# Kernel optimization log

Measured on AMD Instinct MI355X. Metric: run time of the kernel, lower is better.

## Reference

```python
import jax, jax.numpy as jnp
import numpy as np

N_NODES = 100000
N_EDGES = 1600000
F_IN_N = 64
F_IN_E = 64
F_OUT_N = 64
F_OUT_E = 64


def setup_inputs() -> dict:
    key = jax.random.key(0)
    ks = jax.random.split(key, 10)
    nfeats = jax.random.normal(ks[0], (N_NODES, F_IN_N), dtype=jnp.float32)
    efeats = jax.random.normal(ks[1], (N_EDGES, F_IN_E), dtype=jnp.float32)
    src = jax.random.randint(ks[2], (N_EDGES,), 0, N_NODES, dtype=jnp.int32)
    dst = jax.random.randint(ks[3], (N_EDGES,), 0, N_NODES, dtype=jnp.int32)
    s = 0.05
    W_node = jax.random.normal(ks[4], (F_OUT_N, F_IN_N), dtype=jnp.float32) * s
    b_node = jnp.zeros((F_OUT_N,), dtype=jnp.float32)
    W_ni = jax.random.normal(ks[5], (F_OUT_E, F_IN_N), dtype=jnp.float32) * s
    W_nj = jax.random.normal(ks[6], (F_OUT_E, F_IN_N), dtype=jnp.float32) * s
    W_fij = jax.random.normal(ks[7], (F_OUT_E, F_IN_E), dtype=jnp.float32) * s
    bias = jnp.zeros((F_OUT_E,), dtype=jnp.float32)
    return {"nfeats": nfeats, "efeats": efeats, "src": src, "dst": dst,
            "W_node": W_node, "b_node": b_node, "W_ni": W_ni, "W_nj": W_nj,
            "W_fij": W_fij, "bias": bias}


def reference(nfeats, efeats, src, dst, W_node, b_node, W_ni, W_nj, W_fij, bias):
    # edge update: leaky_relu(f_ni[src] + f_nj[dst] + f_fij + bias)
    f_ni = nfeats @ W_ni.T        # [N, Fe]
    f_nj = nfeats @ W_nj.T        # [N, Fe]
    f_fij = efeats @ W_fij.T      # [E, Fe]
    f_out = jax.nn.leaky_relu(f_ni[src] + f_nj[dst] + f_fij + bias, negative_slope=0.01)
    # node update: mean over in-edges of transformed source features
    h = nfeats @ W_node.T + b_node                      # [N, Fn]
    msg_sum = jax.ops.segment_sum(h[src], dst, num_segments=N_NODES)   # [N, Fn]
    deg = jax.ops.segment_sum(jnp.ones((src.shape[0],), dtype=h.dtype), dst,
                              num_segments=N_NODES)
    h_out = msg_sum / jnp.maximum(deg, 1.0)[:, None]    # 0 for isolated nodes
    return (h_out, f_out)
```

## Files before the change

kernel.cpp:

```cpp
#include <hip/hip_runtime.h>

#define NN 100000
#define NE 1600000
#define F 64
#define NSB ((NN + 255) / 256)

typedef float f32x4 __attribute__((ext_vector_type(4)));
typedef short bf16x8 __attribute__((ext_vector_type(8)));

__device__ inline unsigned short f2bf(float f) {
    unsigned u = __builtin_bit_cast(unsigned, f);
    u = (u + 0x7fffu + ((u >> 16) & 1u)) >> 16;
    return (unsigned short)u;
}
__device__ inline float bf2f(unsigned short b) { return __builtin_bit_cast(float, (unsigned)b << 16); }
__device__ inline float bflo(unsigned u) { return __builtin_bit_cast(float, u << 16); }
__device__ inline float bfhi(unsigned u) { return __builtin_bit_cast(float, u & 0xffff0000u); }

__device__ inline bf16x8 pack8(const f32x4 v0, const f32x4 v1) {
    bf16x8 pk;
    pk[0] = (short)f2bf(v0[0]); pk[1] = (short)f2bf(v0[1]);
    pk[2] = (short)f2bf(v0[2]); pk[3] = (short)f2bf(v0[3]);
    pk[4] = (short)f2bf(v1[0]); pk[5] = (short)f2bf(v1[1]);
    pk[6] = (short)f2bf(v1[2]); pk[7] = (short)f2bf(v1[3]);
    return pk;
}

__global__ __launch_bounds__(256, 2) void node_kernel(
    const float* __restrict__ nfeats,
    const float* __restrict__ W_node, const float* __restrict__ b_node,
    const float* __restrict__ W_ni,   const float* __restrict__ W_nj,
    unsigned short* __restrict__ f_ni16, unsigned short* __restrict__ f_nj16,
    unsigned short* __restrict__ h16)
{
    __shared__ bf16x8 As8[256 * 8];
    __shared__ bf16x8 Ws8[3 * 64 * 8];
    float* Df = reinterpret_cast<float*>(As8);

    const int t = threadIdx.x;
    const int w = t >> 6, lane = t & 63;
    const int tile0 = blockIdx.x * 256;

    {
        const float* Wp0 = W_ni; const float* Wp1 = W_nj; const float* Wp2 = W_node;
#pragma unroll
        for (int m = 0; m < 3; ++m) {
            const float* Wp = (m == 0) ? Wp0 : (m == 1) ? Wp1 : Wp2;
            const f32x4* gw = reinterpret_cast<const f32x4*>(Wp);
#pragma unroll
            for (int i = 0; i < 2; ++i) {
                const int c = i * 256 + t;
                const int row = c >> 3, slot = c & 7;
                Ws8[m * 512 + row * 8 + (slot ^ (row & 7))] = pack8(gw[2 * c], gw[2 * c + 1]);
            }
        }
    }
    {
        const f32x4* gsrc = reinterpret_cast<const f32x4*>(nfeats + (size_t)tile0 * F);
#pragma unroll
        for (int i = 0; i < 8; ++i) {
            const int c = i * 256 + t;
            const int row = c >> 3, slot = c & 7;
            f32x4 v0 = f32x4{0.f, 0.f, 0.f, 0.f}, v1 = f32x4{0.f, 0.f, 0.f, 0.f};
            if (tile0 + row < NN) { v0 = gsrc[2 * c]; v1 = gsrc[2 * c + 1]; }
            As8[row * 8 + (slot ^ (row & 7))] = pack8(v0, v1);
        }
    }
    __syncthreads();

    bf16x8 af[4][2];
#pragma unroll
    for (int mt = 0; mt < 4; ++mt)
#pragma unroll
        for (int ks = 0; ks < 2; ++ks) {
            const int row = w * 64 + mt * 16 + (lane & 15);
            const int kslot = ks * 4 + (lane >> 4);
            af[mt][ks] = As8[row * 8 + (kslot ^ (row & 7))];
        }
    __syncthreads();

#pragma unroll
    for (int m = 0; m < 3; ++m) {
        unsigned short* outp = (m == 0) ? f_ni16 : (m == 1) ? f_nj16 : h16;

        bf16x8 bfr[4][2];
#pragma unroll
        for (int nt = 0; nt < 4; ++nt)
#pragma unroll
            for (int ks = 0; ks < 2; ++ks) {
                const int c = nt * 16 + (lane & 15);
                const int kslot = ks * 4 + (lane >> 4);
                bfr[nt][ks] = Ws8[m * 512 + c * 8 + (kslot ^ (c & 7))];
            }

        f32x4 acc[4][4];
#pragma unroll
        for (int mt = 0; mt < 4; ++mt)
#pragma unroll
            for (int nt = 0; nt < 4; ++nt) acc[mt][nt] = f32x4{0.f, 0.f, 0.f, 0.f};
#pragma unroll
        for (int ks = 0; ks < 2; ++ks)
#pragma unroll
            for (int mt = 0; mt < 4; ++mt)
#pragma unroll
                for (int nt = 0; nt < 4; ++nt)
                    acc[mt][nt] = __builtin_amdgcn_mfma_f32_16x16x32_bf16(
                        af[mt][ks], bfr[nt][ks], acc[mt][nt], 0, 0, 0);

#pragma unroll
        for (int half = 0; half < 2; ++half) {
#pragma unroll
            for (int mt = 0; mt < 4; ++mt)
#pragma unroll
                for (int ntl = 0; ntl < 2; ++ntl) {
#pragma unroll
                    for (int r = 0; r < 4; ++r) {
                        const int row = w * 64 + mt * 16 + (lane >> 4) * 4 + r;
                        const int col = ntl * 16 + (lane & 15);
                        float v = acc[mt][half * 2 + ntl][r];
                        if (m == 2) v += b_node[half * 32 + col];
                        Df[row * 32 + ((col + row) & 31)] = v;
                    }
                }
            __syncthreads();

#pragma unroll
            for (int i = 0; i < 4; ++i) {
                const int idx = i * 256 + t;
                const int row = idx >> 2;
                const int c8 = (idx & 3) << 3;
                if (tile0 + row < NN) {
                    const float* b = Df + row * 32;
                    uint4 pk;
                    unsigned u[4];
#pragma unroll
                    for (int p = 0; p < 4; ++p) {
                        const unsigned lo = f2bf(b[(c8 + 2 * p + 0 + row) & 31]);
                        const unsigned hi = f2bf(b[(c8 + 2 * p + 1 + row) & 31]);
                        u[p] = lo | (hi << 16);
                    }
                    pk.x = u[0]; pk.y = u[1]; pk.z = u[2]; pk.w = u[3];
                    *reinterpret_cast<uint4*>(outp + (size_t)(tile0 + row) * F + half * 32 + c8) = pk;
                }
            }
            __syncthreads();
        }
    }
}

__global__ __launch_bounds__(256) void edge_kernel(
    const float* __restrict__ efeats,
    const int* __restrict__ src, const int* __restrict__ dst,
    const unsigned short* __restrict__ f_ni16, const unsigned short* __restrict__ f_nj16,
    const float* __restrict__ W_fij, const float* __restrict__ bias,
    float* __restrict__ f_out)
{
    __shared__ bf16x8 As8[256 * 8];
    __shared__ bf16x8 Ws8[64 * 8];
    float* Df = reinterpret_cast<float*>(As8);

    const int t = threadIdx.x;
    const int w = t >> 6, lane = t & 63;
    const int tile0 = blockIdx.x * 256;
    const int e = tile0 + t;
    const int s = src[e], d = dst[e];

    {
        const f32x4* gw = reinterpret_cast<const f32x4*>(W_fij);
#pragma unroll
        for (int i = 0; i < 2; ++i) {
            const int c = i * 256 + t;
            const int row = c >> 3, slot = c & 7;
            Ws8[row * 8 + (slot ^ (row & 7))] = pack8(gw[2 * c], gw[2 * c + 1]);
        }
    }
    {
        const f32x4* gsrc = reinterpret_cast<const f32x4*>(efeats + (size_t)tile0 * F);
#pragma unroll
        for (int i = 0; i < 8; ++i) {
            const int c = i * 256 + t;
            const int row = c >> 3, slot = c & 7;
            const f32x4 v0 = __builtin_nontemporal_load(gsrc + 2 * c);
            const f32x4 v1 = __builtin_nontemporal_load(gsrc + 2 * c + 1);
            As8[row * 8 + (slot ^ (row & 7))] = pack8(v0, v1);
        }
    }
    const uint4* gi = reinterpret_cast<const uint4*>(f_ni16 + (size_t)s * F);
    const uint4* gj = reinterpret_cast<const uint4*>(f_nj16 + (size_t)d * F);
    uint4 vni[4], vnj[4];
#pragma unroll
    for (int i = 0; i < 4; ++i) { vni[i] = gi[i]; vnj[i] = gj[i]; }

    __syncthreads();

    bf16x8 af[4][2], bfr[4][2];
#pragma unroll
    for (int mt = 0; mt < 4; ++mt)
#pragma unroll
        for (int ks = 0; ks < 2; ++ks) {
            const int row = w * 64 + mt * 16 + (lane & 15);
            const int kslot = ks * 4 + (lane >> 4);
            af[mt][ks] = As8[row * 8 + (kslot ^ (row & 7))];
        }
#pragma unroll
    for (int nt = 0; nt < 4; ++nt)
#pragma unroll
        for (int ks = 0; ks < 2; ++ks) {
            const int c = nt * 16 + (lane & 15);
            const int kslot = ks * 4 + (lane >> 4);
            bfr[nt][ks] = Ws8[c * 8 + (kslot ^ (c & 7))];
        }

    f32x4 acc[4][4];
#pragma unroll
    for (int mt = 0; mt < 4; ++mt)
#pragma unroll
        for (int nt = 0; nt < 4; ++nt) acc[mt][nt] = f32x4{0.f, 0.f, 0.f, 0.f};

#pragma unroll
    for (int ks = 0; ks < 2; ++ks)
#pragma unroll
        for (int mt = 0; mt < 4; ++mt)
#pragma unroll
            for (int nt = 0; nt < 4; ++nt)
                acc[mt][nt] = __builtin_amdgcn_mfma_f32_16x16x32_bf16(
                    af[mt][ks], bfr[nt][ks], acc[mt][nt], 0, 0, 0);

    __syncthreads();

    f32x4* gout = reinterpret_cast<f32x4*>(f_out + (size_t)tile0 * F);

#pragma unroll
    for (int half = 0; half < 2; ++half) {
#pragma unroll
        for (int mt = 0; mt < 4; ++mt)
#pragma unroll
            for (int ntl = 0; ntl < 2; ++ntl) {
                const int nt = half * 2 + ntl;
#pragma unroll
                for (int r = 0; r < 4; ++r) {
                    const int row = w * 64 + mt * 16 + (lane >> 4) * 4 + r;
                    const int col = ntl * 16 + (lane & 15);
                    Df[row * 32 + ((col + row) & 31)] = acc[mt][nt][r];
                }
            }
        uint4 nni[4], nnj[4];
        if (half == 0) {
#pragma unroll
            for (int i = 0; i < 4; ++i) { nni[i] = gi[4 + i]; nnj[i] = gj[4 + i]; }
        }
        __syncthreads();

        float* rb = Df + t * 32;
#pragma unroll
        for (int c = 0; c < 32; ++c) {
            float v = rb[(c + t) & 31];
            const unsigned wi = vni[c >> 3][(c >> 1) & 3];
            const unsigned wj = vnj[c >> 3][(c >> 1) & 3];
            v += (c & 1) ? bfhi(wi) : bflo(wi);
            v += (c & 1) ? bfhi(wj) : bflo(wj);
            v += bias[half * 32 + c];
            v = (v > 0.f) ? v : 0.01f * v;
            rb[(c + t) & 31] = v;
        }
        __syncthreads();

#pragma unroll
        for (int i = 0; i < 8; ++i) {
            const int idx = i * 256 + t;
            const int row = idx >> 3;
            const int c4 = (idx & 7) << 2;
            const float* b = Df + row * 32;
            f32x4 v;
            v[0] = b[(c4 + 0 + row) & 31];
            v[1] = b[(c4 + 1 + row) & 31];
            v[2] = b[(c4 + 2 + row) & 31];
            v[3] = b[(c4 + 3 + row) & 31];
            __builtin_nontemporal_store(v, gout + row * 16 + half * 8 + (idx & 7));
        }
        if (half == 0) {
            __syncthreads();
#pragma unroll
            for (int i = 0; i < 4; ++i) { vni[i] = nni[i]; vnj[i] = nnj[i]; }
        }
    }
}

__global__ __launch_bounds__(256) void hist_kernel(
    const int* __restrict__ dst, int* __restrict__ counts)
{
    const int e = blockIdx.x * 256 + threadIdx.x;
    if (e >= NE) return;
    atomicAdd(&counts[dst[e]], 1);
}

__global__ __launch_bounds__(256) void scan1_kernel(
    const int* __restrict__ counts, int* __restrict__ offsets, int* __restrict__ blocksums)
{
    __shared__ int sd[256];
    const int t = threadIdx.x;
    const int i = blockIdx.x * 256 + t;
    const int v = (i < NN) ? counts[i] : 0;
    sd[t] = v;
    __syncthreads();
#pragma unroll
    for (int off = 1; off < 256; off <<= 1) {
        const int x = (t >= off) ? sd[t - off] : 0;
        __syncthreads();
        sd[t] += x;
        __syncthreads();
    }
    if (i < NN) offsets[i] = sd[t] - v;
    if (t == 255) blocksums[blockIdx.x] = sd[255];
}

__global__ __launch_bounds__(512) void scan2_kernel(
    const int* __restrict__ blocksums, int* __restrict__ blockpref)
{
    __shared__ int sd[512];
    const int t = threadIdx.x;
    const int v = (t < NSB) ? blocksums[t] : 0;
    sd[t] = v;
    __syncthreads();
#pragma unroll
    for (int off = 1; off < 512; off <<= 1) {
        const int x = (t >= off) ? sd[t - off] : 0;
        __syncthreads();
        sd[t] += x;
        __syncthreads();
    }
    if (t < NSB) blockpref[t] = sd[t] - v;
}

__global__ __launch_bounds__(256) void scan3_kernel(
    int* __restrict__ offsets, const int* __restrict__ blockpref, int* __restrict__ cursor)
{
    const int i = blockIdx.x * 256 + threadIdx.x;
    if (i < NN) {
        const int o = offsets[i] + blockpref[blockIdx.x];
        offsets[i] = o;
        cursor[i] = o;
    }
    if (i == 0) offsets[NN] = NE;
}

__global__ __launch_bounds__(256) void place_kernel(
    const int* __restrict__ src, const int* __restrict__ dst,
    int* __restrict__ cursor, int* __restrict__ eidx)
{
    const int e = blockIdx.x * 256 + threadIdx.x;
    if (e >= NE) return;
    const int pos = atomicAdd(&cursor[dst[e]], 1);
    eidx[pos] = src[e];
}

__global__ __launch_bounds__(256) void gather_kernel(
    const unsigned short* __restrict__ h16, const int* __restrict__ offsets,
    const int* __restrict__ eidx, float* __restrict__ h_out)
{
    const int n = blockIdx.x * 4 + (threadIdx.x >> 6);
    const int lane = threadIdx.x & 63;
    if (n >= NN) return;
    const int beg = offsets[n], end = offsets[n + 1];
    float acc = 0.f;
    int k = beg;
    for (; k + 4 <= end; k += 4) {
        const int s0 = eidx[k], s1 = eidx[k + 1], s2 = eidx[k + 2], s3 = eidx[k + 3];
        const float v0 = bf2f(h16[(size_t)s0 * F + lane]);
        const float v1 = bf2f(h16[(size_t)s1 * F + lane]);
        const float v2 = bf2f(h16[(size_t)s2 * F + lane]);
        const float v3 = bf2f(h16[(size_t)s3 * F + lane]);
        acc += v0; acc += v1; acc += v2; acc += v3;
    }
    for (; k < end; ++k) acc += bf2f(h16[(size_t)eidx[k] * F + lane]);
    const float deg = (float)(end - beg);
    __builtin_nontemporal_store(acc / fmaxf(deg, 1.0f), h_out + (size_t)n * F + lane);
}

extern "C" void kernel_launch(void* const* d_in, const int* in_sizes, int n_in,
                              void* d_out, int out_size, void* d_ws, size_t ws_size,
                              hipStream_t stream)
{
    const float* nfeats = (const float*)d_in[0];
    const float* efeats = (const float*)d_in[1];
    const int*   src    = (const int*)  d_in[2];
    const int*   dst    = (const int*)  d_in[3];
    const float* W_node = (const float*)d_in[4];
    const float* b_node = (const float*)d_in[5];
    const float* W_ni   = (const float*)d_in[6];
    const float* W_nj   = (const float*)d_in[7];
    const float* W_fij  = (const float*)d_in[8];
    const float* bias   = (const float*)d_in[9];

    float* h_out = (float*)d_out;
    float* f_out = (float*)d_out + (size_t)NN * F;

    unsigned short* f_ni16 = (unsigned short*)d_ws;
    unsigned short* f_nj16 = f_ni16 + (size_t)NN * F;
    unsigned short* h16    = f_nj16 + (size_t)NN * F;
    int*   offsets = (int*)(h16 + (size_t)NN * F);
    int*   cursor  = offsets + (NN + 1);
    int*   counts  = cursor + NN;
    int*   eidx    = counts + NN;
    int*   blocksums = eidx + NE;
    int*   blockpref = blocksums + NSB;
    const size_t need = ((size_t)3 * NN * F) * sizeof(unsigned short)
                      + ((size_t)(3 * NN + 1) + NE + 2 * NSB) * sizeof(int);
    if (ws_size < need) return;

    hipMemsetAsync(counts, 0, (size_t)NN * sizeof(int), stream);

    node_kernel<<<(NN + 255) / 256, 256, 0, stream>>>(nfeats, W_node, b_node, W_ni, W_nj, f_ni16, f_nj16, h16);
    edge_kernel<<<NE / 256, 256, 0, stream>>>(efeats, src, dst, f_ni16, f_nj16, W_fij, bias, f_out);
    hist_kernel<<<(NE + 255) / 256, 256, 0, stream>>>(dst, counts);
    scan1_kernel<<<NSB, 256, 0, stream>>>(counts, offsets, blocksums);
    scan2_kernel<<<1, 512, 0, stream>>>(blocksums, blockpref);
    scan3_kernel<<<NSB, 256, 0, stream>>>(offsets, blockpref, cursor);
    place_kernel<<<(NE + 255) / 256, 256, 0, stream>>>(src, dst, cursor, eidx);
    gather_kernel<<<(NN + 3) / 4, 256, 0, stream>>>(h16, offsets, eidx, h_out);
}
```

Measured before the change: 484.4 us.

## Split node GEMM across grid y, fuse count zeroing and histogram into kernels

The node kernel now uses 128-row tiles and a second grid dimension that picks one of the three weight matrices, so each block computes a single projection. This raises the block count and cuts per-block shared memory and registers. Zeroing of the degree counts moves into the node kernel, replacing the memset, and the in-degree histogram atomics move into the edge kernel, removing the separate hist launch and its extra read of dst. In exchange, each node tile's features are now read three times, and the edge kernel does atomic adds alongside its main work.

Measured after the change: 432.7 us. 10.7% less time.

```diff
diff --git a/kernel.cpp b/kernel.cpp
--- a/kernel.cpp
+++ b/kernel.cpp
@@ -4,6 +4,7 @@
 #define NE 1600000
 #define F 64
 #define NSB ((NN + 255) / 256)
+#define NTB ((NN + 127) / 128)
 
 typedef float f32x4 __attribute__((ext_vector_type(4)));
 typedef short bf16x8 __attribute__((ext_vector_type(8)));
@@ -31,34 +32,33 @@
     const float* __restrict__ W_node, const float* __restrict__ b_node,
     const float* __restrict__ W_ni,   const float* __restrict__ W_nj,
     unsigned short* __restrict__ f_ni16, unsigned short* __restrict__ f_nj16,
-    unsigned short* __restrict__ h16)
-{
-    __shared__ bf16x8 As8[256 * 8];
-    __shared__ bf16x8 Ws8[3 * 64 * 8];
+    unsigned short* __restrict__ h16, int* __restrict__ counts)
+{
+    __shared__ bf16x8 As8[128 * 8];
+    __shared__ bf16x8 Ws8[64 * 8];
     float* Df = reinterpret_cast<float*>(As8);
 
     const int t = threadIdx.x;
     const int w = t >> 6, lane = t & 63;
-    const int tile0 = blockIdx.x * 256;
+    const int tile0 = blockIdx.x * 128;
+    const int m = blockIdx.y;
+
+    if (m == 0 && t < 128 && tile0 + t < NN) counts[tile0 + t] = 0;
 
     {
-        const float* Wp0 = W_ni; const float* Wp1 = W_nj; const float* Wp2 = W_node;
-#pragma unroll
-        for (int m = 0; m < 3; ++m) {
-            const float* Wp = (m == 0) ? Wp0 : (m == 1) ? Wp1 : Wp2;
-            const f32x4* gw = reinterpret_cast<const f32x4*>(Wp);
-#pragma unroll
-            for (int i = 0; i < 2; ++i) {
-                const int c = i * 256 + t;
-                const int row = c >> 3, slot = c & 7;
-                Ws8[m * 512 + row * 8 + (slot ^ (row & 7))] = pack8(gw[2 * c], gw[2 * c + 1]);
-            }
+        const float* Wp = (m == 0) ? W_ni : (m == 1) ? W_nj : W_node;
+        const f32x4* gw = reinterpret_cast<const f32x4*>(Wp);
+#pragma unroll
+        for (int i = 0; i < 2; ++i) {
+            const int c = i * 256 + t;
+            const int row = c >> 3, slot = c & 7;
+            Ws8[row * 8 + (slot ^ (row & 7))] = pack8(gw[2 * c], gw[2 * c + 1]);
         }
     }
     {
         const f32x4* gsrc = reinterpret_cast<const f32x4*>(nfeats + (size_t)tile0 * F);
 #pragma unroll
-        for (int i = 0; i < 8; ++i) {
+        for (int i = 0; i < 4; ++i) {
             const int c = i * 256 + t;
             const int row = c >> 3, slot = c & 7;
             f32x4 v0 = f32x4{0.f, 0.f, 0.f, 0.f}, v1 = f32x4{0.f, 0.f, 0.f, 0.f};
@@ -68,83 +68,81 @@
     }
     __syncthreads();
 
-    bf16x8 af[4][2];
-#pragma unroll
-    for (int mt = 0; mt < 4; ++mt)
+    bf16x8 af[2][2];
+#pragma unroll
+    for (int mt = 0; mt < 2; ++mt)
 #pragma unroll
         for (int ks = 0; ks < 2; ++ks) {
-            const int row = w * 64 + mt * 16 + (lane & 15);
+            const int row = w * 32 + mt * 16 + (lane & 15);
             const int kslot = ks * 4 + (lane >> 4);
             af[mt][ks] = As8[row * 8 + (kslot ^ (row & 7))];
         }
-    __syncthreads();
-
-#pragma unroll
-    for (int m = 0; m < 3; ++m) {
-        unsigned short* outp = (m == 0) ? f_ni16 : (m == 1) ? f_nj16 : h16;
-
-        bf16x8 bfr[4][2];
-#pragma unroll
-        for (int nt = 0; nt < 4; ++nt)
-#pragma unroll
-            for (int ks = 0; ks < 2; ++ks) {
-                const int c = nt * 16 + (lane & 15);
-                const int kslot = ks * 4 + (lane >> 4);
-                bfr[nt][ks] = Ws8[m * 512 + c * 8 + (kslot ^ (c & 7))];
-            }
-
-        f32x4 acc[4][4];
-#pragma unroll
-        for (int mt = 0; mt < 4; ++mt)
-#pragma unroll
-            for (int nt = 0; nt < 4; ++nt) acc[mt][nt] = f32x4{0.f, 0.f, 0.f, 0.f};
-#pragma unroll
-        for (int ks = 0; ks < 2; ++ks)
-#pragma unroll
-            for (int mt = 0; mt < 4; ++mt)
-#pragma unroll
-                for (int nt = 0; nt < 4; ++nt)
-                    acc[mt][nt] = __builtin_amdgcn_mfma_f32_16x16x32_bf16(
-                        af[mt][ks], bfr[nt][ks], acc[mt][nt], 0, 0, 0);
-
-#pragma unroll
-        for (int half = 0; half < 2; ++half) {
-#pragma unroll
-            for (int mt = 0; mt < 4; ++mt)
-#pragma unroll
-                for (int ntl = 0; ntl < 2; ++ntl) {
-#pragma unroll
-                    for (int r = 0; r < 4; ++r) {
-                        const int row = w * 64 + mt * 16 + (lane >> 4) * 4 + r;
-                        const int col = ntl * 16 + (lane & 15);
-                        float v = acc[mt][half * 2 + ntl][r];
-                        if (m == 2) v += b_node[half * 32 + col];
-                        Df[row * 32 + ((col + row) & 31)] = v;
-                    }
-                }
-            __syncthreads();
-
-#pragma unroll
-            for (int i = 0; i < 4; ++i) {
-                const int idx = i * 256 + t;
-                const int row = idx >> 2;
-                const int c8 = (idx & 3) << 3;
-                if (tile0 + row < NN) {
-                    const float* b = Df + row * 32;
-                    uint4 pk;
-                    unsigned u[4];
-#pragma unroll
-                    for (int p = 0; p < 4; ++p) {
-                        const unsigned lo = f2bf(b[(c8 + 2 * p + 0 + row) & 31]);
-                        const unsigned hi = f2bf(b[(c8 + 2 * p + 1 + row) & 31]);
-                        u[p] = lo | (hi << 16);
-                    }
-                    pk.x = u[0]; pk.y = u[1]; pk.z = u[2]; pk.w = u[3];
-                    *reinterpret_cast<uint4*>(outp + (size_t)(tile0 + row) * F + half * 32 + c8) = pk;
+
+    bf16x8 bfr[4][2];
+#pragma unroll
+    for (int nt = 0; nt < 4; ++nt)
+#pragma unroll
+        for (int ks = 0; ks < 2; ++ks) {
+            const int c = nt * 16 + (lane & 15);
+            const int kslot = ks * 4 + (lane >> 4);
+            bfr[nt][ks] = Ws8[c * 8 + (kslot ^ (c & 7))];
+        }
+
+    f32x4 acc[2][4];
+#pragma unroll
+    for (int mt = 0; mt < 2; ++mt)
+#pragma unroll
+        for (int nt = 0; nt < 4; ++nt) acc[mt][nt] = f32x4{0.f, 0.f, 0.f, 0.f};
+#pragma unroll
+    for (int ks = 0; ks < 2; ++ks)
+#pragma unroll
+        for (int mt = 0; mt < 2; ++mt)
+#pragma unroll
+            for (int nt = 0; nt < 4; ++nt)
+                acc[mt][nt] = __builtin_amdgcn_mfma_f32_16x16x32_bf16(
+                    af[mt][ks], bfr[nt][ks], acc[mt][nt], 0, 0, 0);
+
+    __syncthreads();
+
+    unsigned short* outp = (m == 0) ? f_ni16 : (m == 1) ? f_nj16 : h16;
+
+#pragma unroll
+    for (int half = 0; half < 2; ++half) {
+#pragma unroll
+        for (int mt = 0; mt < 2; ++mt)
+#pragma unroll
+            for (int ntl = 0; ntl < 2; ++ntl) {
+#pragma unroll
+                for (int r = 0; r < 4; ++r) {
+                    const int row = w * 32 + mt * 16 + (lane >> 4) * 4 + r;
+                    const int col = ntl * 16 + (lane & 15);
+                    float v = acc[mt][half * 2 + ntl][r];
+                    if (m == 2) v += b_node[half * 32 + col];
+                    Df[row * 32 + ((col + row) & 31)] = v;
                 }
             }
-            __syncthreads();
-        }
+        __syncthreads();
+
+#pragma unroll
+        for (int i = 0; i < 2; ++i) {
+            const int idx = i * 256 + t;
+            const int row = idx >> 2;
+            const int c8 = (idx & 3) << 3;
+            if (tile0 + row < NN) {
+                const float* b = Df + row * 32;
+                uint4 pk;
+                unsigned u[4];
+#pragma unroll
+                for (int p = 0; p < 4; ++p) {
+                    const unsigned lo = f2bf(b[(c8 + 2 * p + 0 + row) & 31]);
+                    const unsigned hi = f2bf(b[(c8 + 2 * p + 1 + row) & 31]);
+                    u[p] = lo | (hi << 16);
+                }
+                pk.x = u[0]; pk.y = u[1]; pk.z = u[2]; pk.w = u[3];
+                *reinterpret_cast<uint4*>(outp + (size_t)(tile0 + row) * F + half * 32 + c8) = pk;
+            }
+        }
+        __syncthreads();
     }
 }
 
@@ -153,7 +151,7 @@
     const int* __restrict__ src, const int* __restrict__ dst,
     const unsigned short* __restrict__ f_ni16, const unsigned short* __restrict__ f_nj16,
     const float* __restrict__ W_fij, const float* __restrict__ bias,
-    float* __restrict__ f_out)
+    float* __restrict__ f_out, int* __restrict__ counts)
 {
     __shared__ bf16x8 As8[256 * 8];
     __shared__ bf16x8 Ws8[64 * 8];
@@ -164,6 +162,8 @@
     const int tile0 = blockIdx.x * 256;
     const int e = tile0 + t;
     const int s = src[e], d = dst[e];
+
+    atomicAdd(&counts[d], 1);
 
     {
         const f32x4* gw = reinterpret_cast<const f32x4*>(W_fij);
@@ -284,14 +284,6 @@
             for (int i = 0; i < 4; ++i) { vni[i] = nni[i]; vnj[i] = nnj[i]; }
         }
     }
-}
-
-__global__ __launch_bounds__(256) void hist_kernel(
-    const int* __restrict__ dst, int* __restrict__ counts)
-{
-    const int e = blockIdx.x * 256 + threadIdx.x;
-    if (e >= NE) return;
-    atomicAdd(&counts[dst[e]], 1);
 }
 
 __global__ __launch_bounds__(256) void scan1_kernel(
@@ -408,11 +400,10 @@
                       + ((size_t)(3 * NN + 1) + NE + 2 * NSB) * sizeof(int);
     if (ws_size < need) return;
 
-    hipMemsetAsync(counts, 0, (size_t)NN * sizeof(int), stream);
-
-    node_kernel<<<(NN + 255) / 256, 256, 0, stream>>>(nfeats, W_node, b_node, W_ni, W_nj, f_ni16, f_nj16, h16);
-    edge_kernel<<<NE / 256, 256, 0, stream>>>(efeats, src, dst, f_ni16, f_nj16, W_fij, bias, f_out);
-    hist_kernel<<<(NE + 255) / 256, 256, 0, stream>>>(dst, counts);
+    node_kernel<<<dim3(NTB, 3), 256, 0, stream>>>(nfeats, W_node, b_node, W_ni, W_nj,
+                                                  f_ni16, f_nj16, h16, counts);
+    edge_kernel<<<NE / 256, 256, 0, stream>>>(efeats, src, dst, f_ni16, f_nj16, W_fij, bias,
+                                              f_out, counts);
     scan1_kernel<<<NSB, 256, 0, stream>>>(counts, offsets, blocksums);
     scan2_kernel<<<1, 512, 0, stream>>>(blocksums, blockpref);
     scan3_kernel<<<NSB, 256, 0, stream>>>(offsets, blockpref, cursor);
```
